# Performance work log

Hardware: AMD Instinct MI355X
Metric: run time of the kernel (lower is better)

Reference implementation:

```python
import jax, jax.numpy as jnp
import numpy as np


def setup_inputs() -> dict:
    key = jax.random.key(0)
    k1, k2, k3, k4 = jax.random.split(key, 4)
    B, C_in, E = 8, 32, 100000
    C_out, K = 64, 5
    x = jax.random.normal(k1, (B, C_in, E, 1), dtype=jnp.float32)
    gemm_edges = jax.random.randint(k2, (B, E, 4), 0, E, dtype=jnp.int32)
    fan_in = C_in * K
    weight = jax.random.normal(k3, (C_out, C_in, 1, K), dtype=jnp.float32) / np.sqrt(fan_in)
    bias = jax.random.normal(k4, (C_out,), dtype=jnp.float32) * 0.01
    return {"x": x, "gemm_edges": gemm_edges, "weight": weight, "bias": bias}


def reference(x, gemm_edges, weight, bias):
    # x: (B, C, E, 1) edge features; gemm_edges: (B, E, 4) ring-neighbor indices
    xs = x[..., 0]                                   # (B, C, E)
    B, C, E = xs.shape
    # prepend self index -> (B, E, 5); +1 shifts into padded table (slot 0 = zero pad)
    idx_self = jnp.broadcast_to(jnp.arange(E, dtype=gemm_edges.dtype)[None, :, None], (B, E, 1))
    Gi = jnp.concatenate([idx_self, gemm_edges], axis=2) + 1  # (B, E, 5)
    xp = jnp.pad(xs, ((0, 0), (0, 0), (1, 0)))       # (B, C, E+1) with zero column at index 0
    # per-batch gather: f[b, c, e, k] = xp[b, c, Gi[b, e, k]]
    f = jnp.take_along_axis(xp, Gi.reshape(B, 1, E * 5), axis=2).reshape(B, C, E, 5)
    f0, f1, f2, f3, f4 = (f[..., i] for i in range(5))
    # symmetric functions for neighbor-order invariance
    G = jnp.stack([f0, f1 + f3, f2 + f4, jnp.abs(f1 - f3), jnp.abs(f2 - f4)], axis=3)  # (B, C, E, 5)
    # Conv2d kernel (1, 5) == contraction over (C, k), output (B, C_out, E, 1)
    out = jnp.einsum('bcek,ock->boe', G, weight[:, :, 0, :]) + bias[None, :, None]
    return out[..., None]
```

## Files before the change

### kernel.cpp

```cpp
#include <hip/hip_runtime.h>
#include <stdint.h>

#define E_TOTAL 100000
#define B_TOTAL 8
#define CIN 32
#define COUT 64
#define TILES 1563
#define NUNITS 782
#define NBLK 256

typedef float f32x4  __attribute__((ext_vector_type(4)));
typedef int   i32x4  __attribute__((ext_vector_type(4)));
typedef unsigned u32x4 __attribute__((ext_vector_type(4)));
typedef _Float16 h16x8 __attribute__((ext_vector_type(8)));

union HU { u32x4 u; h16x8 h; };

__device__ inline unsigned pkh(float lo, float hi) {
    auto r = __builtin_amdgcn_cvt_pkrtz(lo, hi);
    return __builtin_bit_cast(unsigned, r);
}
__device__ inline h16x8 ash(u32x4 v) { HU x; x.u = v; return x.h; }
__device__ inline h16x8 habsd(h16x8 a, h16x8 b) {
    HU x; x.h = a - b;
#pragma unroll
    for (int i = 0; i < 4; i++) x.u[i] &= 0x7fff7fffu;
    return x.h;
}

__global__ __launch_bounds__(256) void prep_transpose(
    const float* __restrict__ x, unsigned* __restrict__ xt,
    const float* __restrict__ w, unsigned short* __restrict__ wb) {
    const int tid = threadIdx.x;
    if (blockIdx.x >= TILES * 8) {
        for (int idx = tid; idx < 4 * 5 * 64 * 8; idx += 256) {
            int j = idx & 7;
            int lane = (idx >> 3) & 63;
            int tg = idx >> 9;
            int g = tg % 5;
            int t = tg / 5;
            int nn = lane & 15, qq = lane >> 4;
            int o = nn + 16 * t;
            int c = qq * 8 + j;
            _Float16 hv = (_Float16)w[(o * CIN + c) * 5 + g];
            wb[idx] = __builtin_bit_cast(unsigned short, hv);
        }
        return;
    }
    __shared__ float tbuf[CIN][65];
    const int b = blockIdx.x & 7;
    const int e0 = (blockIdx.x >> 3) * 64;
    const int el = tid & 63;
    const int cw = tid >> 6;
#pragma unroll
    for (int i = 0; i < 8; i++) {
        int c = cw * 8 + i;
        int e = e0 + el;
        float v = (e < E_TOTAL)
            ? __builtin_nontemporal_load(x + ((size_t)b * CIN + c) * E_TOTAL + e)
            : 0.f;
        tbuf[c][el] = v;
    }
    __syncthreads();
    const int c2 = tid & 15;
#pragma unroll
    for (int i = 0; i < 4; i++) {
        int el2 = (tid >> 4) * 4 + i;
        int e = e0 + el2;
        if (e < E_TOTAL) {
            xt[((size_t)b * E_TOTAL + e) * 16 + c2] =
                pkh(tbuf[c2 * 2][el2], tbuf[c2 * 2 + 1][el2]);
        }
    }
}

__global__ __launch_bounds__(256) void meshconv_main(
    const unsigned short* __restrict__ xt,
    const int* __restrict__ ge,
    const u32x4* __restrict__ wb,
    const float* __restrict__ bias,
    float* __restrict__ out) {
    __shared__ u32x4 wlds[1280];
    const int tid = threadIdx.x;
    const int lane = tid & 63;
    const int wv = tid >> 6;
    const int b = blockIdx.x & 7;
    const int blk = blockIdx.x >> 3;
    const int n = lane & 15;
    const int q = lane >> 4;
    const int co = q * 8;

#pragma unroll
    for (int k = 0; k < 5; k++) wlds[tid + k * 256] = wb[tid + k * 256];
    __syncthreads();

    const unsigned short* xb = xt + (size_t)b * E_TOTAL * CIN;
    const int* geb = ge + (size_t)b * E_TOTAL * 4;
    float bv[4];
#pragma unroll
    for (int t = 0; t < 4; t++) bv[t] = bias[n + 16 * t];

    int u = blk;
    int e0 = u * 128 + wv * 32;
    bool act = (u < NUNITS) && (e0 < E_TOTAL);
    i32x4 nidA0, nidA1;
    u32x4 sA0, sA1;
    if (act) {
        nidA0 = __builtin_nontemporal_load((const i32x4*)(geb + (size_t)(e0 + n) * 4));
        nidA1 = __builtin_nontemporal_load((const i32x4*)(geb + (size_t)(e0 + 16 + n) * 4));
        sA0 = *(const u32x4*)(xb + (size_t)(e0 + n) * CIN + co);
        sA1 = *(const u32x4*)(xb + (size_t)(e0 + 16 + n) * CIN + co);
    }
    u32x4 g10, g20, g30, g40, g11, g21, g31, g41;
    if (act) {
        g10 = *(const u32x4*)(xb + (size_t)nidA0[0] * CIN + co);
        g20 = *(const u32x4*)(xb + (size_t)nidA0[1] * CIN + co);
        g30 = *(const u32x4*)(xb + (size_t)nidA0[2] * CIN + co);
        g40 = *(const u32x4*)(xb + (size_t)nidA0[3] * CIN + co);
        g11 = *(const u32x4*)(xb + (size_t)nidA1[0] * CIN + co);
        g21 = *(const u32x4*)(xb + (size_t)nidA1[1] * CIN + co);
        g31 = *(const u32x4*)(xb + (size_t)nidA1[2] * CIN + co);
        g41 = *(const u32x4*)(xb + (size_t)nidA1[3] * CIN + co);
    }
    int un = u + NBLK;
    int e0n = un * 128 + wv * 32;
    bool actn = (un < NUNITS) && (e0n < E_TOTAL);
    i32x4 nidB0, nidB1;
    u32x4 sB0, sB1;
    if (actn) {
        nidB0 = __builtin_nontemporal_load((const i32x4*)(geb + (size_t)(e0n + n) * 4));
        nidB1 = __builtin_nontemporal_load((const i32x4*)(geb + (size_t)(e0n + 16 + n) * 4));
        sB0 = *(const u32x4*)(xb + (size_t)(e0n + n) * CIN + co);
        sB1 = *(const u32x4*)(xb + (size_t)(e0n + 16 + n) * CIN + co);
    }

    for (; u < NUNITS; u += NBLK) {
        const int e0c = u * 128 + wv * 32;

        f32x4 acc0[4], acc1[4];
#pragma unroll
        for (int t = 0; t < 4; t++)
#pragma unroll
            for (int r = 0; r < 4; r++) { acc0[t][r] = bv[t]; acc1[t][r] = bv[t]; }

        if (act) {
            {
                HU av0; av0.u = sA0;
                HU av1; av1.u = sA1;
#pragma unroll
                for (int t = 0; t < 4; t++) {
                    HU bw; bw.u = wlds[(t * 5 + 0) * 64 + lane];
                    acc0[t] = __builtin_amdgcn_mfma_f32_16x16x32_f16(av0.h, bw.h, acc0[t], 0, 0, 0);
                    acc1[t] = __builtin_amdgcn_mfma_f32_16x16x32_f16(av1.h, bw.h, acc1[t], 0, 0, 0);
                }
            }
            {
                h16x8 p0 = ash(g10) + ash(g30);
                h16x8 p1 = ash(g11) + ash(g31);
                h16x8 m0 = habsd(ash(g10), ash(g30));
                h16x8 m1 = habsd(ash(g11), ash(g31));
#pragma unroll
                for (int t = 0; t < 4; t++) {
                    HU bw; bw.u = wlds[(t * 5 + 1) * 64 + lane];
                    acc0[t] = __builtin_amdgcn_mfma_f32_16x16x32_f16(p0, bw.h, acc0[t], 0, 0, 0);
                    acc1[t] = __builtin_amdgcn_mfma_f32_16x16x32_f16(p1, bw.h, acc1[t], 0, 0, 0);
                }
#pragma unroll
                for (int t = 0; t < 4; t++) {
                    HU bw; bw.u = wlds[(t * 5 + 3) * 64 + lane];
                    acc0[t] = __builtin_amdgcn_mfma_f32_16x16x32_f16(m0, bw.h, acc0[t], 0, 0, 0);
                    acc1[t] = __builtin_amdgcn_mfma_f32_16x16x32_f16(m1, bw.h, acc1[t], 0, 0, 0);
                }
            }
        }
        if (actn) {
            g10 = *(const u32x4*)(xb + (size_t)nidB0[0] * CIN + co);
            g30 = *(const u32x4*)(xb + (size_t)nidB0[2] * CIN + co);
            g11 = *(const u32x4*)(xb + (size_t)nidB1[0] * CIN + co);
            g31 = *(const u32x4*)(xb + (size_t)nidB1[2] * CIN + co);
        }
        if (act) {
            {
                h16x8 p0 = ash(g20) + ash(g40);
                h16x8 p1 = ash(g21) + ash(g41);
                h16x8 m0 = habsd(ash(g20), ash(g40));
                h16x8 m1 = habsd(ash(g21), ash(g41));
#pragma unroll
                for (int t = 0; t < 4; t++) {
                    HU bw; bw.u = wlds[(t * 5 + 2) * 64 + lane];
                    acc0[t] = __builtin_amdgcn_mfma_f32_16x16x32_f16(p0, bw.h, acc0[t], 0, 0, 0);
                    acc1[t] = __builtin_amdgcn_mfma_f32_16x16x32_f16(p1, bw.h, acc1[t], 0, 0, 0);
                }
#pragma unroll
                for (int t = 0; t < 4; t++) {
                    HU bw; bw.u = wlds[(t * 5 + 4) * 64 + lane];
                    acc0[t] = __builtin_amdgcn_mfma_f32_16x16x32_f16(m0, bw.h, acc0[t], 0, 0, 0);
                    acc1[t] = __builtin_amdgcn_mfma_f32_16x16x32_f16(m1, bw.h, acc1[t], 0, 0, 0);
                }
            }
        }
        if (actn) {
            g20 = *(const u32x4*)(xb + (size_t)nidB0[1] * CIN + co);
            g40 = *(const u32x4*)(xb + (size_t)nidB0[3] * CIN + co);
            g21 = *(const u32x4*)(xb + (size_t)nidB1[1] * CIN + co);
            g41 = *(const u32x4*)(xb + (size_t)nidB1[3] * CIN + co);
        }

        u32x4 sN0 = sB0, sN1 = sB1;
        const int u2 = u + 2 * NBLK;
        const int e02 = u2 * 128 + wv * 32;
        const bool act2 = (u2 < NUNITS) && (e02 < E_TOTAL);
        if (act2) {
            nidB0 = __builtin_nontemporal_load((const i32x4*)(geb + (size_t)(e02 + n) * 4));
            nidB1 = __builtin_nontemporal_load((const i32x4*)(geb + (size_t)(e02 + 16 + n) * 4));
            sB0 = *(const u32x4*)(xb + (size_t)(e02 + n) * CIN + co);
            sB1 = *(const u32x4*)(xb + (size_t)(e02 + 16 + n) * CIN + co);
        }

        if (act) {
#pragma unroll
            for (int t = 0; t < 4; t++) {
                const int o = n + 16 * t;
                float* orow = out + ((size_t)b * COUT + o) * E_TOTAL + e0c + q * 4;
                __builtin_nontemporal_store(acc0[t], (f32x4*)orow);
                __builtin_nontemporal_store(acc1[t], (f32x4*)(orow + 16));
            }
        }

        sA0 = sN0; sA1 = sN1;
        act = actn; actn = act2;
    }
}

__global__ __launch_bounds__(256) void meshconv_fallback(
    const float* __restrict__ x, const int* __restrict__ ge,
    const float* __restrict__ w, const float* __restrict__ bias,
    float* __restrict__ out) {
    __shared__ float f[5][32];
    __shared__ float G[5][32];
    __shared__ int idxs[4];
    const int e = blockIdx.x, b = blockIdx.y;
    const int tid = threadIdx.x;
    if (tid < 4) idxs[tid] = ge[((size_t)b * E_TOTAL + e) * 4 + tid];
    __syncthreads();
    if (tid < 160) {
        int k = tid >> 5, c = tid & 31;
        int src = (k == 0) ? e : idxs[k - 1];
        f[k][c] = x[((size_t)b * CIN + c) * E_TOTAL + src];
    }
    __syncthreads();
    if (tid < 32) {
        int c = tid;
        G[0][c] = f[0][c];
        G[1][c] = f[1][c] + f[3][c];
        G[2][c] = f[2][c] + f[4][c];
        G[3][c] = fabsf(f[1][c] - f[3][c]);
        G[4][c] = fabsf(f[2][c] - f[4][c]);
    }
    __syncthreads();
    if (tid < COUT) {
        float acc = bias[tid];
        for (int c = 0; c < CIN; c++)
#pragma unroll
            for (int g = 0; g < 5; g++)
                acc += G[g][c] * w[(tid * CIN + c) * 5 + g];
        out[((size_t)b * COUT + tid) * E_TOTAL + e] = acc;
    }
}

extern "C" void kernel_launch(void* const* d_in, const int* in_sizes, int n_in,
                              void* d_out, int out_size, void* d_ws, size_t ws_size,
                              hipStream_t stream) {
    const float* x = (const float*)d_in[0];
    const int* ge = (const int*)d_in[1];
    const float* w = (const float*)d_in[2];
    const float* bias = (const float*)d_in[3];
    float* out = (float*)d_out;

    const size_t xt_bytes = (size_t)B_TOTAL * E_TOTAL * CIN * 2;
    const size_t need = 65536 + xt_bytes;
    if (ws_size < need) {
        dim3 grid(E_TOTAL, B_TOTAL);
        meshconv_fallback<<<grid, 256, 0, stream>>>(x, ge, w, bias, out);
        return;
    }
    unsigned short* wb = (unsigned short*)d_ws;
    unsigned short* xt = (unsigned short*)((char*)d_ws + 65536);

    prep_transpose<<<TILES * 8 + 1, 256, 0, stream>>>(x, (unsigned*)xt, w, wb);
    meshconv_main<<<NBLK * 8, 256, 0, stream>>>(xt, ge, (const u32x4*)wb, bias, out);
}
```

Baseline: 375.0 us.

## Replace persistent software-pipelined loop with one block per edge unit

The main kernel stops using a persistent grid of 256 blocks per batch that loops over units with a manual two-stage prefetch of indices and gathers. It now launches one block per 128-edge unit per batch, so each block does one unit. It also issues the index and self-feature loads before the weight copy to LDS and the barrier, so their latency overlaps that copy. Latency hiding now relies on occupancy across many blocks rather than in-thread prefetch, at the cost of reloading the weights into LDS in every block.

```diff
diff --git a/kernel.cpp b/kernel.cpp
--- a/kernel.cpp
+++ b/kernel.cpp
@@ -7,7 +7,6 @@
 #define COUT 64
 #define TILES 1563
 #define NUNITS 782
-#define NBLK 256
 
 typedef float f32x4  __attribute__((ext_vector_type(4)));
 typedef int   i32x4  __attribute__((ext_vector_type(4)));
@@ -85,150 +84,104 @@
     const int lane = tid & 63;
     const int wv = tid >> 6;
     const int b = blockIdx.x & 7;
-    const int blk = blockIdx.x >> 3;
+    const int unit = blockIdx.x >> 3;
     const int n = lane & 15;
     const int q = lane >> 4;
     const int co = q * 8;
 
-#pragma unroll
-    for (int k = 0; k < 5; k++) wlds[tid + k * 256] = wb[tid + k * 256];
-    __syncthreads();
-
     const unsigned short* xb = xt + (size_t)b * E_TOTAL * CIN;
     const int* geb = ge + (size_t)b * E_TOTAL * 4;
+
+    const int e0 = unit * 128 + wv * 32;
+    const bool act = e0 < E_TOTAL;
+
+    i32x4 nid0, nid1;
+    u32x4 s0, s1;
+    if (act) {
+        nid0 = __builtin_nontemporal_load((const i32x4*)(geb + (size_t)(e0 + n) * 4));
+        nid1 = __builtin_nontemporal_load((const i32x4*)(geb + (size_t)(e0 + 16 + n) * 4));
+        s0 = *(const u32x4*)(xb + (size_t)(e0 + n) * CIN + co);
+        s1 = *(const u32x4*)(xb + (size_t)(e0 + 16 + n) * CIN + co);
+    }
     float bv[4];
 #pragma unroll
     for (int t = 0; t < 4; t++) bv[t] = bias[n + 16 * t];
 
-    int u = blk;
-    int e0 = u * 128 + wv * 32;
-    bool act = (u < NUNITS) && (e0 < E_TOTAL);
-    i32x4 nidA0, nidA1;
-    u32x4 sA0, sA1;
-    if (act) {
-        nidA0 = __builtin_nontemporal_load((const i32x4*)(geb + (size_t)(e0 + n) * 4));
-        nidA1 = __builtin_nontemporal_load((const i32x4*)(geb + (size_t)(e0 + 16 + n) * 4));
-        sA0 = *(const u32x4*)(xb + (size_t)(e0 + n) * CIN + co);
-        sA1 = *(const u32x4*)(xb + (size_t)(e0 + 16 + n) * CIN + co);
-    }
+#pragma unroll
+    for (int k = 0; k < 5; k++) wlds[tid + k * 256] = wb[tid + k * 256];
+    __syncthreads();
+
+    if (!act) return;
+
     u32x4 g10, g20, g30, g40, g11, g21, g31, g41;
-    if (act) {
-        g10 = *(const u32x4*)(xb + (size_t)nidA0[0] * CIN + co);
-        g20 = *(const u32x4*)(xb + (size_t)nidA0[1] * CIN + co);
-        g30 = *(const u32x4*)(xb + (size_t)nidA0[2] * CIN + co);
-        g40 = *(const u32x4*)(xb + (size_t)nidA0[3] * CIN + co);
-        g11 = *(const u32x4*)(xb + (size_t)nidA1[0] * CIN + co);
-        g21 = *(const u32x4*)(xb + (size_t)nidA1[1] * CIN + co);
-        g31 = *(const u32x4*)(xb + (size_t)nidA1[2] * CIN + co);
-        g41 = *(const u32x4*)(xb + (size_t)nidA1[3] * CIN + co);
-    }
-    int un = u + NBLK;
-    int e0n = un * 128 + wv * 32;
-    bool actn = (un < NUNITS) && (e0n < E_TOTAL);
-    i32x4 nidB0, nidB1;
-    u32x4 sB0, sB1;
-    if (actn) {
-        nidB0 = __builtin_nontemporal_load((const i32x4*)(geb + (size_t)(e0n + n) * 4));
-        nidB1 = __builtin_nontemporal_load((const i32x4*)(geb + (size_t)(e0n + 16 + n) * 4));
-        sB0 = *(const u32x4*)(xb + (size_t)(e0n + n) * CIN + co);
-        sB1 = *(const u32x4*)(xb + (size_t)(e0n + 16 + n) * CIN + co);
-    }
-
-    for (; u < NUNITS; u += NBLK) {
-        const int e0c = u * 128 + wv * 32;
-
-        f32x4 acc0[4], acc1[4];
-#pragma unroll
-        for (int t = 0; t < 4; t++)
-#pragma unroll
-            for (int r = 0; r < 4; r++) { acc0[t][r] = bv[t]; acc1[t][r] = bv[t]; }
-
-        if (act) {
-            {
-                HU av0; av0.u = sA0;
-                HU av1; av1.u = sA1;
-#pragma unroll
-                for (int t = 0; t < 4; t++) {
-                    HU bw; bw.u = wlds[(t * 5 + 0) * 64 + lane];
-                    acc0[t] = __builtin_amdgcn_mfma_f32_16x16x32_f16(av0.h, bw.h, acc0[t], 0, 0, 0);
-                    acc1[t] = __builtin_amdgcn_mfma_f32_16x16x32_f16(av1.h, bw.h, acc1[t], 0, 0, 0);
-                }
-            }
-            {
-                h16x8 p0 = ash(g10) + ash(g30);
-                h16x8 p1 = ash(g11) + ash(g31);
-                h16x8 m0 = habsd(ash(g10), ash(g30));
-                h16x8 m1 = habsd(ash(g11), ash(g31));
-#pragma unroll
-                for (int t = 0; t < 4; t++) {
-                    HU bw; bw.u = wlds[(t * 5 + 1) * 64 + lane];
-                    acc0[t] = __builtin_amdgcn_mfma_f32_16x16x32_f16(p0, bw.h, acc0[t], 0, 0, 0);
-                    acc1[t] = __builtin_amdgcn_mfma_f32_16x16x32_f16(p1, bw.h, acc1[t], 0, 0, 0);
-                }
-#pragma unroll
-                for (int t = 0; t < 4; t++) {
-                    HU bw; bw.u = wlds[(t * 5 + 3) * 64 + lane];
-                    acc0[t] = __builtin_amdgcn_mfma_f32_16x16x32_f16(m0, bw.h, acc0[t], 0, 0, 0);
-                    acc1[t] = __builtin_amdgcn_mfma_f32_16x16x32_f16(m1, bw.h, acc1[t], 0, 0, 0);
-                }
-            }
-        }
-        if (actn) {
-            g10 = *(const u32x4*)(xb + (size_t)nidB0[0] * CIN + co);
-            g30 = *(const u32x4*)(xb + (size_t)nidB0[2] * CIN + co);
-            g11 = *(const u32x4*)(xb + (size_t)nidB1[0] * CIN + co);
-            g31 = *(const u32x4*)(xb + (size_t)nidB1[2] * CIN + co);
-        }
-        if (act) {
-            {
-                h16x8 p0 = ash(g20) + ash(g40);
-                h16x8 p1 = ash(g21) + ash(g41);
-                h16x8 m0 = habsd(ash(g20), ash(g40));
-                h16x8 m1 = habsd(ash(g21), ash(g41));
-#pragma unroll
-                for (int t = 0; t < 4; t++) {
-                    HU bw; bw.u = wlds[(t * 5 + 2) * 64 + lane];
-                    acc0[t] = __builtin_amdgcn_mfma_f32_16x16x32_f16(p0, bw.h, acc0[t], 0, 0, 0);
-                    acc1[t] = __builtin_amdgcn_mfma_f32_16x16x32_f16(p1, bw.h, acc1[t], 0, 0, 0);
-                }
-#pragma unroll
-                for (int t = 0; t < 4; t++) {
-                    HU bw; bw.u = wlds[(t * 5 + 4) * 64 + lane];
-                    acc0[t] = __builtin_amdgcn_mfma_f32_16x16x32_f16(m0, bw.h, acc0[t], 0, 0, 0);
-                    acc1[t] = __builtin_amdgcn_mfma_f32_16x16x32_f16(m1, bw.h, acc1[t], 0, 0, 0);
-                }
-            }
-        }
-        if (actn) {
-            g20 = *(const u32x4*)(xb + (size_t)nidB0[1] * CIN + co);
-            g40 = *(const u32x4*)(xb + (size_t)nidB0[3] * CIN + co);
-            g21 = *(const u32x4*)(xb + (size_t)nidB1[1] * CIN + co);
-            g41 = *(const u32x4*)(xb + (size_t)nidB1[3] * CIN + co);
-        }
-
-        u32x4 sN0 = sB0, sN1 = sB1;
-        const int u2 = u + 2 * NBLK;
-        const int e02 = u2 * 128 + wv * 32;
-        const bool act2 = (u2 < NUNITS) && (e02 < E_TOTAL);
-        if (act2) {
-            nidB0 = __builtin_nontemporal_load((const i32x4*)(geb + (size_t)(e02 + n) * 4));
-            nidB1 = __builtin_nontemporal_load((const i32x4*)(geb + (size_t)(e02 + 16 + n) * 4));
-            sB0 = *(const u32x4*)(xb + (size_t)(e02 + n) * CIN + co);
-            sB1 = *(const u32x4*)(xb + (size_t)(e02 + 16 + n) * CIN + co);
-        }
-
-        if (act) {
-#pragma unroll
-            for (int t = 0; t < 4; t++) {
-                const int o = n + 16 * t;
-                float* orow = out + ((size_t)b * COUT + o) * E_TOTAL + e0c + q * 4;
-                __builtin_nontemporal_store(acc0[t], (f32x4*)orow);
-                __builtin_nontemporal_store(acc1[t], (f32x4*)(orow + 16));
-            }
-        }
-
-        sA0 = sN0; sA1 = sN1;
-        act = actn; actn = act2;
+    g10 = *(const u32x4*)(xb + (size_t)nid0[0] * CIN + co);
+    g20 = *(const u32x4*)(xb + (size_t)nid0[1] * CIN + co);
+    g30 = *(const u32x4*)(xb + (size_t)nid0[2] * CIN + co);
+    g40 = *(const u32x4*)(xb + (size_t)nid0[3] * CIN + co);
+    g11 = *(const u32x4*)(xb + (size_t)nid1[0] * CIN + co);
+    g21 = *(const u32x4*)(xb + (size_t)nid1[1] * CIN + co);
+    g31 = *(const u32x4*)(xb + (size_t)nid1[2] * CIN + co);
+    g41 = *(const u32x4*)(xb + (size_t)nid1[3] * CIN + co);
+
+    f32x4 acc0[4], acc1[4];
+#pragma unroll
+    for (int t = 0; t < 4; t++)
+#pragma unroll
+        for (int r = 0; r < 4; r++) { acc0[t][r] = bv[t]; acc1[t][r] = bv[t]; }
+
+    {
+        HU av0; av0.u = s0;
+        HU av1; av1.u = s1;
+#pragma unroll
+        for (int t = 0; t < 4; t++) {
+            HU bw; bw.u = wlds[(t * 5 + 0) * 64 + lane];
+            acc0[t] = __builtin_amdgcn_mfma_f32_16x16x32_f16(av0.h, bw.h, acc0[t], 0, 0, 0);
+            acc1[t] = __builtin_amdgcn_mfma_f32_16x16x32_f16(av1.h, bw.h, acc1[t], 0, 0, 0);
+        }
+    }
+    {
+        h16x8 p0 = ash(g10) + ash(g30);
+        h16x8 p1 = ash(g11) + ash(g31);
+        h16x8 m0 = habsd(ash(g10), ash(g30));
+        h16x8 m1 = habsd(ash(g11), ash(g31));
+#pragma unroll
+        for (int t = 0; t < 4; t++) {
+            HU bw; bw.u = wlds[(t * 5 + 1) * 64 + lane];
+            acc0[t] = __builtin_amdgcn_mfma_f32_16x16x32_f16(p0, bw.h, acc0[t], 0, 0, 0);
+            acc1[t] = __builtin_amdgcn_mfma_f32_16x16x32_f16(p1, bw.h, acc1[t], 0, 0, 0);
+        }
+#pragma unroll
+        for (int t = 0; t < 4; t++) {
+            HU bw; bw.u = wlds[(t * 5 + 3) * 64 + lane];
+            acc0[t] = __builtin_amdgcn_mfma_f32_16x16x32_f16(m0, bw.h, acc0[t], 0, 0, 0);
+            acc1[t] = __builtin_amdgcn_mfma_f32_16x16x32_f16(m1, bw.h, acc1[t], 0, 0, 0);
+        }
+    }
+    {
+        h16x8 p0 = ash(g20) + ash(g40);
+        h16x8 p1 = ash(g21) + ash(g41);
+        h16x8 m0 = habsd(ash(g20), ash(g40));
+        h16x8 m1 = habsd(ash(g21), ash(g41));
+#pragma unroll
+        for (int t = 0; t < 4; t++) {
+            HU bw; bw.u = wlds[(t * 5 + 2) * 64 + lane];
+            acc0[t] = __builtin_amdgcn_mfma_f32_16x16x32_f16(p0, bw.h, acc0[t], 0, 0, 0);
+            acc1[t] = __builtin_amdgcn_mfma_f32_16x16x32_f16(p1, bw.h, acc1[t], 0, 0, 0);
+        }
+#pragma unroll
+        for (int t = 0; t < 4; t++) {
+            HU bw; bw.u = wlds[(t * 5 + 4) * 64 + lane];
+            acc0[t] = __builtin_amdgcn_mfma_f32_16x16x32_f16(m0, bw.h, acc0[t], 0, 0, 0);
+            acc1[t] = __builtin_amdgcn_mfma_f32_16x16x32_f16(m1, bw.h, acc1[t], 0, 0, 0);
+        }
+    }
+
+#pragma unroll
+    for (int t = 0; t < 4; t++) {
+        const int o = n + 16 * t;
+        float* orow = out + ((size_t)b * COUT + o) * E_TOTAL + e0 + q * 4;
+        __builtin_nontemporal_store(acc0[t], (f32x4*)orow);
+        __builtin_nontemporal_store(acc1[t], (f32x4*)(orow + 16));
     }
 }
 
@@ -288,5 +241,5 @@
     unsigned short* xt = (unsigned short*)((char*)d_ws + 65536);
 
     prep_transpose<<<TILES * 8 + 1, 256, 0, stream>>>(x, (unsigned*)xt, w, wb);
-    meshconv_main<<<NBLK * 8, 256, 0, stream>>>(xt, ge, (const u32x4*)wb, bias, out);
-}
+    meshconv_main<<<NUNITS * 8, 256, 0, stream>>>(xt, ge, (const u32x4*)wb, bias, out);
+}
```

Result: no change. 372.7 us (-0.6%).
